# Performance work log

Measured on AMD Instinct MI355X. Metric: run time of the kernel, lower is better.

Reference implementation:

```python
import jax, jax.numpy as jnp
import numpy as np

B, S, H = 64, 1024, 1000

def setup_inputs() -> dict:
    key = jax.random.key(0)
    k1, k2, k3, k4 = jax.random.split(key, 4)
    h_tgt = jax.random.normal(k1, (B, 1, H), dtype=jnp.float32)
    h_src = jax.random.normal(k2, (B, S, H), dtype=jnp.float32)
    # nn.Linear(H, H) params: weight [H, H], bias [H]
    bound = 1.0 / np.sqrt(H)
    W = jax.random.uniform(k3, (H, H), dtype=jnp.float32, minval=-bound, maxval=bound)
    b = jax.random.uniform(k4, (H,), dtype=jnp.float32, minval=-bound, maxval=bound)
    return {"h_tgt": h_tgt, "h_src": h_src, "W": W, "b": b}

def reference(h_tgt, h_src, W, b):
    # score[b,t] = h_tgt[b,0] . (W @ h_src[b,t] + bias)  -- Luong general attention
    proj = jnp.einsum('bsh,gh->bsg', h_src, W) + b          # [B,S,H]
    score = jnp.einsum('bh,bsh->bs', h_tgt[:, 0], proj)      # [B,S]
    a = jax.nn.softmax(score, axis=1)                        # [B,S]
    c = jnp.einsum('bs,bsh->bh', a, h_src)[:, None, :]       # [B,1,H]
    return c
```

## Files before the change

### kernel.cpp

```cpp
#include <hip/hip_runtime.h>

constexpr int Bb = 64;
constexpr int Ss = 1024;
constexpr int Hh = 1000;
constexpr int CHUNKS = 32;
constexpr int CS = Ss / CHUNKS;

__global__ __launch_bounds__(256) void proj_tgt_kernel(
    const float* __restrict__ h_tgt, const float* __restrict__ W,
    float* __restrict__ u)
{
    const int h = blockIdx.x * blockDim.x + threadIdx.x;
    const int b = blockIdx.y;
    if (h >= Hh) return;
    const float* ht = h_tgt + b * Hh;
    float acc = 0.f;
    #pragma unroll 8
    for (int g = 0; g < Hh; ++g)
        acc = fmaf(ht[g], W[g * Hh + h], acc);
    u[b * Hh + h] = acc;
}

__global__ __launch_bounds__(256) void attn_partial_kernel(
    const float* __restrict__ h_src, const float* __restrict__ u,
    float* __restrict__ wsM, float* __restrict__ wsL, float* __restrict__ wsC)
{
    const int lane  = threadIdx.x & 63;
    const int wave  = (int)((blockIdx.x * blockDim.x + threadIdx.x) >> 6);
    const int b     = wave / CHUNKS;
    const int chunk = wave % CHUNKS;
    const int s0    = chunk * CS;

    const float* ub = u + b * Hh;
    float4 uf[4];
    #pragma unroll
    for (int j = 0; j < 4; ++j) {
        const int d = j * 256 + lane * 4;
        uf[j] = (d < Hh) ? *(const float4*)(ub + d) : make_float4(0.f, 0.f, 0.f, 0.f);
    }

    float m = -INFINITY, l = 0.f;
    float4 c[4];
    #pragma unroll
    for (int j = 0; j < 4; ++j) c[j] = make_float4(0.f, 0.f, 0.f, 0.f);

    const float* xp = h_src + (size_t)(b * Ss + s0) * Hh;
    for (int s = 0; s < CS; ++s) {
        float4 x[4];
        #pragma unroll
        for (int j = 0; j < 4; ++j) {
            const int d = j * 256 + lane * 4;
            x[j] = (d < Hh) ? *(const float4*)(xp + d) : make_float4(0.f, 0.f, 0.f, 0.f);
        }
        float part = 0.f;
        #pragma unroll
        for (int j = 0; j < 4; ++j) {
            part = fmaf(x[j].x, uf[j].x, part);
            part = fmaf(x[j].y, uf[j].y, part);
            part = fmaf(x[j].z, uf[j].z, part);
            part = fmaf(x[j].w, uf[j].w, part);
        }
        #pragma unroll
        for (int off = 32; off > 0; off >>= 1)
            part += __shfl_xor(part, off, 64);
        const float score = part;

        if (score > m) {
            const float scale = __expf(m - score);
            m = score;
            l *= scale;
            #pragma unroll
            for (int j = 0; j < 4; ++j) {
                c[j].x *= scale; c[j].y *= scale; c[j].z *= scale; c[j].w *= scale;
            }
        }
        const float p = __expf(score - m);
        l += p;
        #pragma unroll
        for (int j = 0; j < 4; ++j) {
            c[j].x = fmaf(p, x[j].x, c[j].x);
            c[j].y = fmaf(p, x[j].y, c[j].y);
            c[j].z = fmaf(p, x[j].z, c[j].z);
            c[j].w = fmaf(p, x[j].w, c[j].w);
        }
        xp += Hh;
    }

    const int idx = b * CHUNKS + chunk;
    if (lane == 0) { wsM[idx] = m; wsL[idx] = l; }
    float* cw = wsC + (size_t)idx * Hh;
    #pragma unroll
    for (int j = 0; j < 4; ++j) {
        const int d = j * 256 + lane * 4;
        if (d < Hh) *(float4*)(cw + d) = c[j];
    }
}

__global__ __launch_bounds__(256) void combine_kernel(
    const float* __restrict__ wsM, const float* __restrict__ wsL,
    const float* __restrict__ wsC, float* __restrict__ out)
{
    const int b = blockIdx.x;
    __shared__ float sw[CHUNKS];
    __shared__ float sInvL;
    if (threadIdx.x == 0) {
        float M = -INFINITY;
        for (int i = 0; i < CHUNKS; ++i) M = fmaxf(M, wsM[b * CHUNKS + i]);
        float L = 0.f;
        for (int i = 0; i < CHUNKS; ++i) {
            const float e = __expf(wsM[b * CHUNKS + i] - M);
            sw[i] = e;
            L = fmaf(e, wsL[b * CHUNKS + i], L);
        }
        sInvL = 1.f / L;
    }
    __syncthreads();
    for (int h = (int)threadIdx.x; h < Hh; h += (int)blockDim.x) {
        float acc = 0.f;
        #pragma unroll 8
        for (int i = 0; i < CHUNKS; ++i)
            acc = fmaf(sw[i], wsC[(size_t)(b * CHUNKS + i) * Hh + h], acc);
        out[b * Hh + h] = acc * sInvL;
    }
}

extern "C" void kernel_launch(void* const* d_in, const int* in_sizes, int n_in,
                              void* d_out, int out_size, void* d_ws, size_t ws_size,
                              hipStream_t stream) {
    const float* h_tgt = (const float*)d_in[0];
    const float* h_src = (const float*)d_in[1];
    const float* W     = (const float*)d_in[2];
    float* out = (float*)d_out;

    float* u   = (float*)d_ws;
    float* wsM = u + Bb * Hh;
    float* wsL = wsM + Bb * CHUNKS;
    float* wsC = wsL + Bb * CHUNKS;

    proj_tgt_kernel<<<dim3((Hh + 255) / 256, Bb), 256, 0, stream>>>(h_tgt, W, u);
    attn_partial_kernel<<<(Bb * CHUNKS) / 4, 256, 0, stream>>>(h_src, u, wsM, wsL, wsC);
    combine_kernel<<<Bb, 256, 0, stream>>>(wsM, wsL, wsC, out);
}
```

Before: 438.2 us.

## Restructure all three kernels for more parallelism and memory-level overlap

The target projection kernel now handles 4 batches per block and splits the reduction dimension across 4 waves with a shared-memory reduction, so each W element is reused across batches. The attention kernel doubles the split of the sequence into 64 chunks and processes two rows per iteration to put more loads in flight. The combine kernel replaces the serial single-thread softmax merge with wave shuffles and spreads the H dimension over 4 blocks per batch. These changes aim to raise occupancy and bandwidth use, at the cost of a larger partial workspace and more combine traffic.

```diff
diff --git a/kernel.cpp b/kernel.cpp
--- a/kernel.cpp
+++ b/kernel.cpp
@@ -3,22 +3,44 @@
 constexpr int Bb = 64;
 constexpr int Ss = 1024;
 constexpr int Hh = 1000;
-constexpr int CHUNKS = 32;
+constexpr int CHUNKS = 64;
 constexpr int CS = Ss / CHUNKS;
+constexpr int BG = 4;
+constexpr int GQ = 4;
 
 __global__ __launch_bounds__(256) void proj_tgt_kernel(
     const float* __restrict__ h_tgt, const float* __restrict__ W,
     float* __restrict__ u)
 {
-    const int h = blockIdx.x * blockDim.x + threadIdx.x;
-    const int b = blockIdx.y;
-    if (h >= Hh) return;
-    const float* ht = h_tgt + b * Hh;
-    float acc = 0.f;
-    #pragma unroll 8
-    for (int g = 0; g < Hh; ++g)
-        acc = fmaf(ht[g], W[g * Hh + h], acc);
-    u[b * Hh + h] = acc;
+    const int hl = threadIdx.x & 63;
+    const int gq = threadIdx.x >> 6;
+    const int h  = blockIdx.x * 64 + hl;
+    const int b0 = blockIdx.y * BG;
+    const bool hok = (h < Hh);
+
+    float acc[BG] = {0.f, 0.f, 0.f, 0.f};
+    const int g0 = gq * (Hh / GQ);
+    const int g1 = g0 + (Hh / GQ);
+    #pragma unroll 2
+    for (int g = g0; g < g1; ++g) {
+        const float w = hok ? W[g * Hh + h] : 0.f;
+        #pragma unroll
+        for (int bi = 0; bi < BG; ++bi)
+            acc[bi] = fmaf(h_tgt[(b0 + bi) * Hh + g], w, acc[bi]);
+    }
+
+    __shared__ float red[GQ][BG][64];
+    #pragma unroll
+    for (int bi = 0; bi < BG; ++bi) red[gq][bi][hl] = acc[bi];
+    __syncthreads();
+    if (gq == 0 && hok) {
+        #pragma unroll
+        for (int bi = 0; bi < BG; ++bi) {
+            const float s = red[0][bi][hl] + red[1][bi][hl]
+                          + red[2][bi][hl] + red[3][bi][hl];
+            u[(b0 + bi) * Hh + h] = s;
+        }
+    }
 }
 
 __global__ __launch_bounds__(256) void attn_partial_kernel(
@@ -27,8 +49,8 @@
 {
     const int lane  = threadIdx.x & 63;
     const int wave  = (int)((blockIdx.x * blockDim.x + threadIdx.x) >> 6);
-    const int b     = wave / CHUNKS;
-    const int chunk = wave % CHUNKS;
+    const int b     = wave >> 6;
+    const int chunk = wave & 63;
     const int s0    = chunk * CS;
 
     const float* ub = u + b * Hh;
@@ -45,45 +67,51 @@
     for (int j = 0; j < 4; ++j) c[j] = make_float4(0.f, 0.f, 0.f, 0.f);
 
     const float* xp = h_src + (size_t)(b * Ss + s0) * Hh;
-    for (int s = 0; s < CS; ++s) {
-        float4 x[4];
+    #pragma unroll 2
+    for (int s = 0; s < CS; s += 2) {
+        float4 x0[4], x1[4];
         #pragma unroll
         for (int j = 0; j < 4; ++j) {
             const int d = j * 256 + lane * 4;
-            x[j] = (d < Hh) ? *(const float4*)(xp + d) : make_float4(0.f, 0.f, 0.f, 0.f);
+            x0[j] = (d < Hh) ? *(const float4*)(xp + d)      : make_float4(0.f,0.f,0.f,0.f);
+            x1[j] = (d < Hh) ? *(const float4*)(xp + Hh + d) : make_float4(0.f,0.f,0.f,0.f);
         }
-        float part = 0.f;
+        float p0 = 0.f, p1 = 0.f;
         #pragma unroll
         for (int j = 0; j < 4; ++j) {
-            part = fmaf(x[j].x, uf[j].x, part);
-            part = fmaf(x[j].y, uf[j].y, part);
-            part = fmaf(x[j].z, uf[j].z, part);
-            part = fmaf(x[j].w, uf[j].w, part);
+            p0 = fmaf(x0[j].x, uf[j].x, p0); p0 = fmaf(x0[j].y, uf[j].y, p0);
+            p0 = fmaf(x0[j].z, uf[j].z, p0); p0 = fmaf(x0[j].w, uf[j].w, p0);
+            p1 = fmaf(x1[j].x, uf[j].x, p1); p1 = fmaf(x1[j].y, uf[j].y, p1);
+            p1 = fmaf(x1[j].z, uf[j].z, p1); p1 = fmaf(x1[j].w, uf[j].w, p1);
         }
         #pragma unroll
-        for (int off = 32; off > 0; off >>= 1)
-            part += __shfl_xor(part, off, 64);
-        const float score = part;
+        for (int off = 32; off > 0; off >>= 1) {
+            p0 += __shfl_xor(p0, off, 64);
+            p1 += __shfl_xor(p1, off, 64);
+        }
+        const float sc0 = p0, sc1 = p1;
 
-        if (score > m) {
-            const float scale = __expf(m - score);
-            m = score;
+        const float mn = fmaxf(m, fmaxf(sc0, sc1));
+        if (mn > m) {
+            const float scale = __expf(m - mn);
+            m = mn;
             l *= scale;
             #pragma unroll
             for (int j = 0; j < 4; ++j) {
                 c[j].x *= scale; c[j].y *= scale; c[j].z *= scale; c[j].w *= scale;
             }
         }
-        const float p = __expf(score - m);
-        l += p;
+        const float e0 = __expf(sc0 - m);
+        const float e1 = __expf(sc1 - m);
+        l += e0 + e1;
         #pragma unroll
         for (int j = 0; j < 4; ++j) {
-            c[j].x = fmaf(p, x[j].x, c[j].x);
-            c[j].y = fmaf(p, x[j].y, c[j].y);
-            c[j].z = fmaf(p, x[j].z, c[j].z);
-            c[j].w = fmaf(p, x[j].w, c[j].w);
+            c[j].x = fmaf(e0, x0[j].x, fmaf(e1, x1[j].x, c[j].x));
+            c[j].y = fmaf(e0, x0[j].y, fmaf(e1, x1[j].y, c[j].y));
+            c[j].z = fmaf(e0, x0[j].z, fmaf(e1, x1[j].z, c[j].z));
+            c[j].w = fmaf(e0, x0[j].w, fmaf(e1, x1[j].w, c[j].w));
         }
-        xp += Hh;
+        xp += 2 * Hh;
     }
 
     const int idx = b * CHUNKS + chunk;
@@ -100,22 +128,28 @@
     const float* __restrict__ wsM, const float* __restrict__ wsL,
     const float* __restrict__ wsC, float* __restrict__ out)
 {
-    const int b = blockIdx.x;
+    const int b   = blockIdx.x;
+    const int tid = (int)threadIdx.x;
     __shared__ float sw[CHUNKS];
     __shared__ float sInvL;
-    if (threadIdx.x == 0) {
-        float M = -INFINITY;
-        for (int i = 0; i < CHUNKS; ++i) M = fmaxf(M, wsM[b * CHUNKS + i]);
-        float L = 0.f;
-        for (int i = 0; i < CHUNKS; ++i) {
-            const float e = __expf(wsM[b * CHUNKS + i] - M);
-            sw[i] = e;
-            L = fmaf(e, wsL[b * CHUNKS + i], L);
-        }
-        sInvL = 1.f / L;
+
+    if (tid < 64) {
+        const float mi = wsM[b * CHUNKS + tid];
+        const float li = wsL[b * CHUNKS + tid];
+        float M = mi;
+        #pragma unroll
+        for (int off = 32; off > 0; off >>= 1) M = fmaxf(M, __shfl_xor(M, off, 64));
+        const float w = __expf(mi - M);
+        float L = w * li;
+        #pragma unroll
+        for (int off = 32; off > 0; off >>= 1) L += __shfl_xor(L, off, 64);
+        sw[tid] = w;
+        if (tid == 0) sInvL = 1.f / L;
     }
     __syncthreads();
-    for (int h = (int)threadIdx.x; h < Hh; h += (int)blockDim.x) {
+
+    const int h = blockIdx.y * 250 + tid;
+    if (tid < 250) {
         float acc = 0.f;
         #pragma unroll 8
         for (int i = 0; i < CHUNKS; ++i)
@@ -137,7 +171,7 @@
     float* wsL = wsM + Bb * CHUNKS;
     float* wsC = wsL + Bb * CHUNKS;
 
-    proj_tgt_kernel<<<dim3((Hh + 255) / 256, Bb), 256, 0, stream>>>(h_tgt, W, u);
+    proj_tgt_kernel<<<dim3((Hh + 63) / 64, Bb / BG), 256, 0, stream>>>(h_tgt, W, u);
     attn_partial_kernel<<<(Bb * CHUNKS) / 4, 256, 0, stream>>>(h_src, u, wsM, wsL, wsC);
-    combine_kernel<<<Bb, 256, 0, stream>>>(wsM, wsL, wsC, out);
+    combine_kernel<<<dim3(Bb, 4), 256, 0, stream>>>(wsM, wsL, wsC, out);
 }
```

New measurement: 429.8 us. About the same (-1.9%).
